# Kernel optimization log

Hardware: AMD Instinct MI355X
Metric: run time of the kernel (lower is better)

Reference implementation:

```python
import jax, jax.numpy as jnp
import numpy as np

INPUT_DIM = 1024
LATENT_DIM = 1024


def setup_inputs() -> dict:
    key = jax.random.key(0)
    ks = jax.random.split(key, 8)
    B, T = 64, 512
    concat_dim = INPUT_DIM + LATENT_DIM
    s = lambda fan_in: 1.0 / np.sqrt(fan_in)
    return {
        "x": jax.random.normal(ks[0], (B, T, INPUT_DIM), dtype=jnp.float32),
        "h0": jax.random.normal(ks[1], (B, LATENT_DIM), dtype=jnp.float32),
        "w_W": jax.random.uniform(ks[2], (concat_dim, 2 * LATENT_DIM), jnp.float32, -s(concat_dim), s(concat_dim)),
        "w_b": jax.random.uniform(ks[3], (2 * LATENT_DIM,), jnp.float32, -s(concat_dim), s(concat_dim)),
        "wx_W": jax.random.uniform(ks[4], (INPUT_DIM, LATENT_DIM), jnp.float32, -s(INPUT_DIM), s(INPUT_DIM)),
        "wx_b": jax.random.uniform(ks[5], (LATENT_DIM,), jnp.float32, -s(INPUT_DIM), s(INPUT_DIM)),
        "wh_W": jax.random.uniform(ks[6], (LATENT_DIM, LATENT_DIM), jnp.float32, -s(LATENT_DIM), s(LATENT_DIM)),
        "wh_b": jax.random.uniform(ks[7], (LATENT_DIM,), jnp.float32, -s(LATENT_DIM), s(LATENT_DIM)),
    }


def reference(x, h0, w_W, w_b, wx_W, wx_b, wh_W, wh_b):
    # x: [B, T, D_in] (batch_first). Scan over time.
    xT = jnp.swapaxes(x, 0, 1)  # [T, B, D_in]

    def step(h, x_t):
        # fused gate: sigmoid(cat([x,h]) @ W + b) -> chunk into hidden/output gates
        fused = jax.nn.sigmoid(jnp.concatenate([x_t, h], axis=-1) @ w_W + w_b)
        hidden_state, output_state = jnp.split(fused, 2, axis=-1)
        memory_state = (x_t @ wx_W + wx_b) + hidden_state * (h @ wh_W + wh_b)
        h_new = output_state * h + (1.0 - output_state) * jnp.tanh(memory_state)
        return h_new, h_new

    _, hs = jax.lax.scan(step, h0, xT)  # hs: [T, B, L]
    return jnp.swapaxes(hs, 0, 1)  # [B, T, L]
```

## Files before the change

### kernel.cpp

```cpp
#include <hip/hip_runtime.h>
#include <hip/hip_bf16.h>


typedef __attribute__((ext_vector_type(4))) int   int4v;
typedef __attribute__((ext_vector_type(4))) short short4v;
typedef __attribute__((ext_vector_type(8))) short bf16x8;
typedef __attribute__((ext_vector_type(4))) float f32x4;

union Pack16 { int4v i; short4v s[2]; };
union FragU  { bf16x8 v; short4v s[2]; int4v i; };

__device__ __forceinline__ short f2bf(float f) {
  union { float f; unsigned u; } v; v.f = f;
  unsigned r = v.u + 0x7fffu + ((v.u >> 16) & 1u);
  return (short)(r >> 16);
}
__device__ __forceinline__ float bf2f(short s) {
  union { unsigned u; float f; } v; v.u = ((unsigned)(unsigned short)s) << 16;
  return v.f;
}


__global__ __launch_bounds__(256) void cast_x_kernel(const float* __restrict__ xf,
                                                     short* __restrict__ xbf, int n4) {
  int i = blockIdx.x * 256 + threadIdx.x;
  if (i < n4) {
    float4 v = ((const float4*)xf)[i];
    short4v o;
    o.x = f2bf(v.x); o.y = f2bf(v.y); o.z = f2bf(v.z); o.w = f2bf(v.w);
    int r_in = i >> 8, c = i & 255;
    int b = r_in >> 9, t = r_in & 511;
    ((short4v*)xbf)[((t << 6) + b) * 256 + c] = o;
  }
}

__global__ __launch_bounds__(256) void transpose_cast(const float* __restrict__ src,
                                                      long ld, short* __restrict__ dst) {
  __shared__ float tile[64][65];
  const int n0 = blockIdx.x << 6, k0 = blockIdx.y << 6;
  const int c = threadIdx.x & 63, rr = threadIdx.x >> 6;
#pragma unroll 4
  for (int i = 0; i < 16; ++i)
    tile[i * 4 + rr][c] = src[(long)(k0 + i * 4 + rr) * ld + n0 + c];
  __syncthreads();
#pragma unroll 4
  for (int i = 0; i < 16; ++i)
    dst[(long)(n0 + i * 4 + rr) * 1024 + k0 + c] = f2bf(tile[c][i * 4 + rr]);
}

__global__ __launch_bounds__(256) void prep_misc(const float* __restrict__ wb,
                                                 const float* __restrict__ wxb,
                                                 const float* __restrict__ h0,
                                                 float* __restrict__ biasP,
                                                 short* __restrict__ hbf0) {
  int i = blockIdx.x * 256 + threadIdx.x;
  if (i < 65536) {
    hbf0[i] = f2bf(h0[i]);
  } else {
    int n = i - 65536;
    if (n < 3072) biasP[n] = (n < 2048) ? wb[n] : wxb[n - 2048];
  }
}

__global__ __launch_bounds__(256) void pgemm_kernel(const short* __restrict__ A,
                                                    const short* __restrict__ Bt,
                                                    const float* __restrict__ biasP,
                                                    short* __restrict__ P) {
  __shared__ short As[128][36];
  __shared__ short Bs[128][36];
  const int tid = threadIdx.x;
  const int m0 = blockIdx.y << 7;
  const int n0 = blockIdx.x << 7;
  const int w = tid >> 6, lane = tid & 63;
  const int wm = w >> 1, wn = w & 1;
  const int q = lane >> 4, r = lane & 15;
  const int srow = tid >> 1, shalf = tid & 1;

  const f32x4 zero = {0.f, 0.f, 0.f, 0.f};
  f32x4 acc[4][4];
#pragma unroll
  for (int a = 0; a < 4; ++a)
#pragma unroll
    for (int b = 0; b < 4; ++b) acc[a][b] = zero;

  const short* gA = A + (long)(m0 + srow) * 1024 + shalf * 16;
  const short* gB = Bt + (long)(n0 + srow) * 1024 + shalf * 16;

  for (int kk = 0; kk < 1024; kk += 32) {
    Pack16 a0, a1, b0, b1;
    a0.i = *(const int4v*)(gA + kk);
    a1.i = *(const int4v*)(gA + kk + 8);
    b0.i = *(const int4v*)(gB + kk);
    b1.i = *(const int4v*)(gB + kk + 8);
    short* wA = &As[srow][shalf * 16];
    *(short4v*)(wA)      = a0.s[0];
    *(short4v*)(wA + 4)  = a0.s[1];
    *(short4v*)(wA + 8)  = a1.s[0];
    *(short4v*)(wA + 12) = a1.s[1];
    short* wB = &Bs[srow][shalf * 16];
    *(short4v*)(wB)      = b0.s[0];
    *(short4v*)(wB + 4)  = b0.s[1];
    *(short4v*)(wB + 8)  = b1.s[0];
    *(short4v*)(wB + 12) = b1.s[1];
    __syncthreads();

    FragU af[4], bfv[4];
#pragma unroll
    for (int mi = 0; mi < 4; ++mi) {
      const short* pa = &As[wm * 64 + mi * 16 + r][q * 8];
      af[mi].s[0] = *(const short4v*)pa;
      af[mi].s[1] = *(const short4v*)(pa + 4);
    }
#pragma unroll
    for (int ni = 0; ni < 4; ++ni) {
      const short* pb = &Bs[wn * 64 + ni * 16 + r][q * 8];
      bfv[ni].s[0] = *(const short4v*)pb;
      bfv[ni].s[1] = *(const short4v*)(pb + 4);
    }
#pragma unroll
    for (int mi = 0; mi < 4; ++mi)
#pragma unroll
      for (int ni = 0; ni < 4; ++ni)
        acc[mi][ni] = __builtin_amdgcn_mfma_f32_16x16x32_bf16(af[mi].v, bfv[ni].v,
                                                              acc[mi][ni], 0, 0, 0);
    __syncthreads();
  }

#pragma unroll
  for (int ni = 0; ni < 4; ++ni) {
    int gn = n0 + wn * 64 + ni * 16 + r;
    float bias = biasP[gn];
#pragma unroll
    for (int mi = 0; mi < 4; ++mi) {
      int gm = m0 + wm * 64 + mi * 16 + q * 4;
#pragma unroll
      for (int i = 0; i < 4; ++i)
        P[(long)(gm + i) * 3072 + gn] = f2bf(acc[mi][ni][i] + bias);
    }
  }
}

__global__ __launch_bounds__(256, 1) void recur_kernel(const short* __restrict__ RT,
                                                       const short* __restrict__ P,
                                                       const float* __restrict__ whb,
                                                       const float* __restrict__ h0,
                                                       short* __restrict__ hbuf,
                                                       float* __restrict__ out,
                                                       unsigned* __restrict__ sync) {
  __shared__ float Lred[4][3][256];
  __shared__ unsigned long long hstage_u[32];
  short* hstage = (short*)hstage_u;

  const int tid = threadIdx.x;
  const int bid = blockIdx.x;
  const int cg = bid & 63, bg = bid >> 6;
  const int w = tid >> 6, lane = tid & 63;
  const int q = lane >> 4, r = lane & 15;
  const int ks = w << 8;
  const f32x4 zero = {0.f, 0.f, 0.f, 0.f};

  FragU Bf[3][8];
#pragma unroll
  for (int nt = 0; nt < 3; ++nt)
#pragma unroll
    for (int ki = 0; ki < 8; ++ki) {
      const short* p = RT + (long)(nt * 1024 + cg * 16 + r) * 1024 + ks + ki * 32 + q * 8;
      Pack16 t16; t16.i = *(const int4v*)p;
      Bf[nt][ki].s[0] = t16.s[0]; Bf[nt][ki].s[1] = t16.s[1];
    }

  const int bl = tid >> 4, jl = tid & 15;
  float hp = h0[(long)(bg * 16 + bl) * 1024 + cg * 16 + jl];
  const float whbr = whb[cg * 16 + jl];
  const short* Pbase = P + (long)(bg * 16 + bl) * 3072 + cg * 16 + jl;
  short p0n = Pbase[0], p1n = Pbase[1024], p2n = Pbase[2048];
  const long outbase = ((long)(bg * 16 + bl) * 512) * 1024 + cg * 16 + jl;
  unsigned* gf = sync + 65536 + bg * 32;

  for (int t = 0; t < 512; ++t) {
    const short* hcur = hbuf + (t & 1) * 65536;
    short* hnext = hbuf + ((t + 1) & 1) * 65536;

    const short* aptr = hcur + (bg * 16 + r) * 1024 + ks + q * 8;
    FragU Af[8];
    asm volatile(
        "global_load_dwordx4 %0, %8, off sc0 sc1\n\t"
        "global_load_dwordx4 %1, %8, off offset:64 sc0 sc1\n\t"
        "global_load_dwordx4 %2, %8, off offset:128 sc0 sc1\n\t"
        "global_load_dwordx4 %3, %8, off offset:192 sc0 sc1\n\t"
        "global_load_dwordx4 %4, %8, off offset:256 sc0 sc1\n\t"
        "global_load_dwordx4 %5, %8, off offset:320 sc0 sc1\n\t"
        "global_load_dwordx4 %6, %8, off offset:384 sc0 sc1\n\t"
        "global_load_dwordx4 %7, %8, off offset:448 sc0 sc1\n\t"
        "s_waitcnt vmcnt(0)"
        : "=&v"(Af[0].i), "=&v"(Af[1].i), "=&v"(Af[2].i), "=&v"(Af[3].i),
          "=&v"(Af[4].i), "=&v"(Af[5].i), "=&v"(Af[6].i), "=&v"(Af[7].i)
        : "v"(aptr)
        : "memory");

    short c0 = p0n, c1 = p1n, c2 = p2n;
    if (t < 511) {
      const short* Pn = Pbase + (long)(t + 1) * 196608;
      p0n = Pn[0]; p1n = Pn[1024]; p2n = Pn[2048];
    }

    f32x4 acc0 = zero, acc1 = zero, acc2 = zero;
#pragma unroll
    for (int ki = 0; ki < 8; ++ki) {
      acc0 = __builtin_amdgcn_mfma_f32_16x16x32_bf16(Af[ki].v, Bf[0][ki].v, acc0, 0, 0, 0);
      acc1 = __builtin_amdgcn_mfma_f32_16x16x32_bf16(Af[ki].v, Bf[1][ki].v, acc1, 0, 0, 0);
      acc2 = __builtin_amdgcn_mfma_f32_16x16x32_bf16(Af[ki].v, Bf[2][ki].v, acc2, 0, 0, 0);
    }

#pragma unroll
    for (int i = 0; i < 4; ++i) {
      Lred[w][0][(q * 4 + i) * 16 + r] = acc0[i];
      Lred[w][1][(q * 4 + i) * 16 + r] = acc1[i];
      Lred[w][2][(q * 4 + i) * 16 + r] = acc2[i];
    }
    __syncthreads();

    float g0 = Lred[0][0][tid] + Lred[1][0][tid] + Lred[2][0][tid] + Lred[3][0][tid];
    float g1 = Lred[0][1][tid] + Lred[1][1][tid] + Lred[2][1][tid] + Lred[3][1][tid];
    float g2 = Lred[0][2][tid] + Lred[1][2][tid] + Lred[2][2][tid] + Lred[3][2][tid];

    float gh = 1.f / (1.f + __expf(-(bf2f(c0) + g0)));
    float go = 1.f / (1.f + __expf(-(bf2f(c1) + g1)));
    float mem = bf2f(c2) + gh * (g2 + whbr);
    float e = __expf(2.f * mem);
    float th = 1.f - 2.f / (e + 1.f);
    float hn = go * hp + (1.f - go) * th;
    hp = hn;
    out[outbase + (long)t * 1024] = hn;
    hstage[tid] = f2bf(hn);
    __syncthreads();

    if (tid < 64) {
      int row = bg * 16 + (tid >> 2);
      unsigned long long* hp64 = (unsigned long long*)(hnext + row * 1024 + cg * 16 + (tid & 3) * 4);
      __hip_atomic_store(hp64, hstage_u[tid], __ATOMIC_RELAXED, __HIP_MEMORY_SCOPE_AGENT);
      asm volatile("s_waitcnt vmcnt(0)" ::: "memory");
      if (tid == 0) {
        unsigned* ctr = sync + ((unsigned)t * 4 + bg) * 32;
        unsigned old = __hip_atomic_fetch_add(ctr, 1u, __ATOMIC_RELAXED,
                                              __HIP_MEMORY_SCOPE_AGENT);
        if (old == 63u)
          __hip_atomic_store(gf, (unsigned)(t + 1), __ATOMIC_RELAXED,
                             __HIP_MEMORY_SCOPE_AGENT);
      }
    }
    while (__hip_atomic_load(gf, __ATOMIC_RELAXED, __HIP_MEMORY_SCOPE_AGENT) <
           (unsigned)(t + 1))
      __builtin_amdgcn_s_sleep(1);
  }
}


extern "C" void kernel_launch(void* const* d_in, const int* in_sizes, int n_in,
                              void* d_out, int out_size, void* d_ws, size_t ws_size,
                              hipStream_t stream) {
  const float* x   = (const float*)d_in[0];
  const float* h0  = (const float*)d_in[1];
  const float* wW  = (const float*)d_in[2];
  const float* wb  = (const float*)d_in[3];
  const float* wxW = (const float*)d_in[4];
  const float* wxb = (const float*)d_in[5];
  const float* whW = (const float*)d_in[6];
  const float* whb = (const float*)d_in[7];
  float* out = (float*)d_out;

  char* ws = (char*)d_ws;
  short*    P     = (short*)(ws);
  short*    xbf   = (short*)(ws + 201326592);
  short*    XwT   = (short*)(ws + 268435456);
  short*    RT    = (short*)(ws + 274726912);
  float*    biasP = (float*)(ws + 281018368);
  short*    hbf   = (short*)(ws + 281030656);
  unsigned* sync  = (unsigned*)(ws + 281292800);

  hipMemsetAsync(sync, 0, 262656, stream);
  cast_x_kernel<<<dim3(32768), dim3(256), 0, stream>>>(x, xbf, 8388608);
  transpose_cast<<<dim3(32, 16), dim3(256), 0, stream>>>(wW, 2048, XwT);
  transpose_cast<<<dim3(16, 16), dim3(256), 0, stream>>>(wxW, 1024, XwT + 2048 * 1024);
  transpose_cast<<<dim3(32, 16), dim3(256), 0, stream>>>(wW + 1024 * 2048, 2048, RT);
  transpose_cast<<<dim3(16, 16), dim3(256), 0, stream>>>(whW, 1024, RT + 2048 * 1024);
  prep_misc<<<dim3(268), dim3(256), 0, stream>>>(wb, wxb, h0, biasP, hbf);
  pgemm_kernel<<<dim3(24, 256), dim3(256), 0, stream>>>(xbf, XwT, biasP, P);
  recur_kernel<<<dim3(256), dim3(256), 0, stream>>>(RT, P, whb, h0, hbf, out, sync);
}
```

Before: 2.638 ms.

## Replace counter-based grid barrier with per-block flags and overlap loads with MFMA

Replaces the per-step atomic fetch-add counter plus last-arriver flag with one flag per column-group block. Each block publishes its timestep, and waiters poll all 64 flags of their batch group in parallel using a wave-wide vote. The h loads are split so the first half of the MFMAs start after four of eight loads arrive. The output store and next-step P loads are moved after the flag publish, so they overlap the wait. This aims to cut barrier latency on the serial recurrence, at the cost of more polling traffic.

```diff
diff --git a/kernel.cpp b/kernel.cpp
--- a/kernel.cpp
+++ b/kernel.cpp
@@ -175,7 +175,9 @@
   const short* Pbase = P + (long)(bg * 16 + bl) * 3072 + cg * 16 + jl;
   short p0n = Pbase[0], p1n = Pbase[1024], p2n = Pbase[2048];
   const long outbase = ((long)(bg * 16 + bl) * 512) * 1024 + cg * 16 + jl;
-  unsigned* gf = sync + 65536 + bg * 32;
+
+  unsigned* flagbase = sync + (bg << 6);
+  const unsigned* myflag = flagbase + (w << 4) + (lane & 15);
 
   for (int t = 0; t < 512; ++t) {
     const short* hcur = hbuf + (t & 1) * 65536;
@@ -192,21 +194,23 @@
         "global_load_dwordx4 %5, %8, off offset:320 sc0 sc1\n\t"
         "global_load_dwordx4 %6, %8, off offset:384 sc0 sc1\n\t"
         "global_load_dwordx4 %7, %8, off offset:448 sc0 sc1\n\t"
-        "s_waitcnt vmcnt(0)"
+        "s_waitcnt vmcnt(4)"
         : "=&v"(Af[0].i), "=&v"(Af[1].i), "=&v"(Af[2].i), "=&v"(Af[3].i),
           "=&v"(Af[4].i), "=&v"(Af[5].i), "=&v"(Af[6].i), "=&v"(Af[7].i)
         : "v"(aptr)
         : "memory");
 
-    short c0 = p0n, c1 = p1n, c2 = p2n;
-    if (t < 511) {
-      const short* Pn = Pbase + (long)(t + 1) * 196608;
-      p0n = Pn[0]; p1n = Pn[1024]; p2n = Pn[2048];
-    }
-
     f32x4 acc0 = zero, acc1 = zero, acc2 = zero;
 #pragma unroll
-    for (int ki = 0; ki < 8; ++ki) {
+    for (int ki = 0; ki < 4; ++ki) {
+      acc0 = __builtin_amdgcn_mfma_f32_16x16x32_bf16(Af[ki].v, Bf[0][ki].v, acc0, 0, 0, 0);
+      acc1 = __builtin_amdgcn_mfma_f32_16x16x32_bf16(Af[ki].v, Bf[1][ki].v, acc1, 0, 0, 0);
+      acc2 = __builtin_amdgcn_mfma_f32_16x16x32_bf16(Af[ki].v, Bf[2][ki].v, acc2, 0, 0, 0);
+    }
+    asm volatile("s_waitcnt vmcnt(0)" ::: "memory");
+    __builtin_amdgcn_sched_barrier(0);
+#pragma unroll
+    for (int ki = 4; ki < 8; ++ki) {
       acc0 = __builtin_amdgcn_mfma_f32_16x16x32_bf16(Af[ki].v, Bf[0][ki].v, acc0, 0, 0, 0);
       acc1 = __builtin_amdgcn_mfma_f32_16x16x32_bf16(Af[ki].v, Bf[1][ki].v, acc1, 0, 0, 0);
       acc2 = __builtin_amdgcn_mfma_f32_16x16x32_bf16(Af[ki].v, Bf[2][ki].v, acc2, 0, 0, 0);
@@ -224,14 +228,13 @@
     float g1 = Lred[0][1][tid] + Lred[1][1][tid] + Lred[2][1][tid] + Lred[3][1][tid];
     float g2 = Lred[0][2][tid] + Lred[1][2][tid] + Lred[2][2][tid] + Lred[3][2][tid];
 
-    float gh = 1.f / (1.f + __expf(-(bf2f(c0) + g0)));
-    float go = 1.f / (1.f + __expf(-(bf2f(c1) + g1)));
-    float mem = bf2f(c2) + gh * (g2 + whbr);
+    float gh = 1.f / (1.f + __expf(-(bf2f(p0n) + g0)));
+    float go = 1.f / (1.f + __expf(-(bf2f(p1n) + g1)));
+    float mem = bf2f(p2n) + gh * (g2 + whbr);
     float e = __expf(2.f * mem);
     float th = 1.f - 2.f / (e + 1.f);
     float hn = go * hp + (1.f - go) * th;
     hp = hn;
-    out[outbase + (long)t * 1024] = hn;
     hstage[tid] = f2bf(hn);
     __syncthreads();
 
@@ -240,18 +243,22 @@
       unsigned long long* hp64 = (unsigned long long*)(hnext + row * 1024 + cg * 16 + (tid & 3) * 4);
       __hip_atomic_store(hp64, hstage_u[tid], __ATOMIC_RELAXED, __HIP_MEMORY_SCOPE_AGENT);
       asm volatile("s_waitcnt vmcnt(0)" ::: "memory");
-      if (tid == 0) {
-        unsigned* ctr = sync + ((unsigned)t * 4 + bg) * 32;
-        unsigned old = __hip_atomic_fetch_add(ctr, 1u, __ATOMIC_RELAXED,
-                                              __HIP_MEMORY_SCOPE_AGENT);
-        if (old == 63u)
-          __hip_atomic_store(gf, (unsigned)(t + 1), __ATOMIC_RELAXED,
-                             __HIP_MEMORY_SCOPE_AGENT);
+      if (tid == 0)
+        __hip_atomic_store(flagbase + cg, (unsigned)(t + 1), __ATOMIC_RELAXED,
+                           __HIP_MEMORY_SCOPE_AGENT);
+    }
+
+    out[outbase + (long)t * 1024] = hn;
+    if (t < 511) {
+      const short* Pn = Pbase + (long)(t + 1) * 196608;
+      p0n = Pn[0]; p1n = Pn[1024]; p2n = Pn[2048];
+
+      for (;;) {
+        unsigned f = __hip_atomic_load(myflag, __ATOMIC_RELAXED, __HIP_MEMORY_SCOPE_AGENT);
+        if (__all((int)(f >= (unsigned)(t + 1)))) break;
+        __builtin_amdgcn_s_sleep(1);
       }
     }
-    while (__hip_atomic_load(gf, __ATOMIC_RELAXED, __HIP_MEMORY_SCOPE_AGENT) <
-           (unsigned)(t + 1))
-      __builtin_amdgcn_s_sleep(1);
   }
 }
 
@@ -278,7 +285,7 @@
   short*    hbf   = (short*)(ws + 281030656);
   unsigned* sync  = (unsigned*)(ws + 281292800);
 
-  hipMemsetAsync(sync, 0, 262656, stream);
+  hipMemsetAsync(sync, 0, 1024, stream);
   cast_x_kernel<<<dim3(32768), dim3(256), 0, stream>>>(x, xbf, 8388608);
   transpose_cast<<<dim3(32, 16), dim3(256), 0, stream>>>(wW, 2048, XwT);
   transpose_cast<<<dim3(16, 16), dim3(256), 0, stream>>>(wxW, 1024, XwT + 2048 * 1024);
```

After: 3.134 ms. +18.8%, slower.
